# Kernel tuning notes

Hardware: AMD Instinct MI355X
Metric: run time of the kernel (lower is better)

## Reference

```python
import jax, jax.numpy as jnp
import numpy as np

B, S, D, H = 2, 2048, 1024, 16
DK = D // H


def setup_inputs() -> dict:
    key = jax.random.key(0)
    ks = jax.random.split(key, 9)
    sc = 0.02
    return {
        "x": jax.random.normal(ks[0], (B, S, D), dtype=jnp.float32),
        "attention_mask": jnp.ones((B, S), dtype=jnp.int32),
        "Wq": jax.random.normal(ks[1], (D, D), dtype=jnp.float32) * sc,
        "bq": jax.random.normal(ks[2], (D,), dtype=jnp.float32) * sc,
        "Wk": jax.random.normal(ks[3], (D, D), dtype=jnp.float32) * sc,
        "bk": jax.random.normal(ks[4], (D,), dtype=jnp.float32) * sc,
        "Wv": jax.random.normal(ks[5], (D, D), dtype=jnp.float32) * sc,
        "bv": jax.random.normal(ks[6], (D,), dtype=jnp.float32) * sc,
        "Wo": jax.random.normal(ks[7], (D, D), dtype=jnp.float32) * sc,
        "bo": jax.random.normal(ks[8], (D,), dtype=jnp.float32) * sc,
    }


def reference(x, attention_mask, Wq, bq, Wk, bk, Wv, bv, Wo, bo):
    b, s, d = x.shape
    # projections (Linear: x @ W + b) then split heads -> [b, h, s, dk]
    def heads(t):
        return t.reshape(b, s, H, DK).transpose(0, 2, 1, 3)
    Q = heads(x @ Wq + bq)
    K = heads(x @ Wk + bk)
    V = heads(x @ Wv + bv)
    # NOTE: original computes K @ Q^T (not Q @ K^T) and applies NO 1/sqrt(dk) scale
    scores = jnp.einsum("bhid,bhjd->bhij", K, Q)  # [b, h, s, s]
    causal = jnp.tril(jnp.ones((s, s), dtype=bool))  # [s, s]
    final_mask = attention_mask[:, None, None, :].astype(bool) & causal[None, None]
    scores = jnp.where(final_mask, scores, -jnp.inf)
    attn = jax.nn.softmax(scores, axis=-1)
    out = jnp.einsum("bhij,bhjd->bhid", attn, V)  # [b, h, s, dk]
    out = out.transpose(0, 2, 1, 3).reshape(b, s, d)
    return out @ Wo + bo
```

## Files before the change

### kernel.cpp

```cpp
#include <hip/hip_runtime.h>
#include <stdint.h>
#include <stddef.h>


typedef short bf16x8 __attribute__((ext_vector_type(8)));
typedef float f32x4  __attribute__((ext_vector_type(4)));

__device__ __forceinline__ short f2bf(float f) {
  union { float f; uint32_t u; } a; a.f = f;
  uint32_t r = a.u + 0x7fffu + ((a.u >> 16) & 1u);
  return (short)(r >> 16);
}
__device__ __forceinline__ float bf2f(short s) {
  union { uint32_t u; float f; } a; a.u = ((uint32_t)(uint16_t)s) << 16;
  return a.f;
}
__device__ __forceinline__ uint32_t pack2bf(float a, float b) {
  union { float f; uint32_t u; } x, y; x.f = a; y.f = b;
  return (x.u >> 16) | (y.u & 0xffff0000u);
}
__device__ __forceinline__ float fast_exp2(float x) {
#if __has_builtin(__builtin_amdgcn_exp2f)
  return __builtin_amdgcn_exp2f(x);
#else
  return exp2f(x);
#endif
}
__device__ __forceinline__ void async16(const void* g, void* l) {
  __builtin_amdgcn_global_load_lds(
      (const __attribute__((address_space(1))) uint32_t*)g,
      (__attribute__((address_space(3))) uint32_t*)l, 16, 0, 0);
}
#define MFMA(a, b, c) __builtin_amdgcn_mfma_f32_16x16x32_bf16((a), (b), (c), 0, 0, 0)

__global__ void k_prep(const float* __restrict__ x, short* __restrict__ xhi,
                       const float* __restrict__ Wq, const float* __restrict__ Wk,
                       const float* __restrict__ Wv, const float* __restrict__ Wo,
                       short* __restrict__ whi, short* __restrict__ wo) {
  __shared__ float T[64][65];
  int bid = blockIdx.x;
  int t = threadIdx.x;
  if (bid < 4096) {
    int i = bid * 256 + t;
    float4 v = ((const float4*)x)[i];
    short4 h;
    h.x = f2bf(v.x);
    h.y = f2bf(v.y);
    h.z = f2bf(v.z);
    h.w = f2bf(v.w);
    ((short4*)xhi)[i] = h;
  } else {
    int i = bid - 4096;
    int bx = i & 15, by = (i >> 4) & 15, z = i >> 8;
    const float* W = (z == 0) ? Wq : (z == 1) ? Wk : (z == 2) ? Wv : Wo;
    int n0 = bx * 64, k0 = by * 64;
    int rr = t >> 4, cc = (t & 15) * 4;
#pragma unroll
    for (int it = 0; it < 4; ++it) {
      int row = rr + it * 16;
      float4 v = *(const float4*)&W[(size_t)(k0 + row) * 1024 + n0 + cc];
      T[row][cc] = v.x; T[row][cc + 1] = v.y; T[row][cc + 2] = v.z; T[row][cc + 3] = v.w;
    }
    __syncthreads();
    short* oh = (z < 3) ? (whi + (size_t)z * 1048576) : wo;
#pragma unroll
    for (int it = 0; it < 4; ++it) {
      int nrow = rr + it * 16;
      short4 h4;
      h4.x = f2bf(T[cc + 0][nrow]);
      h4.y = f2bf(T[cc + 1][nrow]);
      h4.z = f2bf(T[cc + 2][nrow]);
      h4.w = f2bf(T[cc + 3][nrow]);
      *(short4*)&oh[(size_t)(n0 + nrow) * 1024 + k0 + cc] = h4;
    }
  }
}

__global__ __launch_bounds__(256, 3) void k_gemm_qkv(
    const short* __restrict__ xhi, const short* __restrict__ whi,
    const float* __restrict__ bq, const float* __restrict__ bk,
    const float* __restrict__ bv,
    short* __restrict__ Qhi, short* __restrict__ Qlo,
    short* __restrict__ Khi, short* __restrict__ Klo,
    short* __restrict__ Vt) {
  __shared__ short AH[2][4096];
  __shared__ short BH[2][4096];
  int tid = threadIdx.x;
  int bx = blockIdx.x;
  int m0 = blockIdx.y * 128;
  int n0g = bx * 128;
  int w = tid >> 6, lane = tid & 63, lr = lane & 15, lq = lane >> 4;
  int wm = w >> 1, wn = w & 1;
  int z = bx >> 3;
  f32x4 acc[4][4] = {};

  auto stage = [&](int ks, int pb) {
#pragma unroll
    for (int it = 0; it < 2; ++it) {
      int idx = it * 256 + tid;
      int row = idx >> 2, c = idx & 3;
      int cs = c ^ (row & 3);
      async16(xhi + (size_t)(m0 + row) * 1024 + ks * 32 + cs * 8, &AH[pb][idx * 8]);
      async16(whi + (size_t)(n0g + row) * 1024 + ks * 32 + cs * 8, &BH[pb][idx * 8]);
    }
  };

  stage(0, 0);
  int p = 0;
  int g = lq ^ (lr & 3);
  if (z == 2) {
    for (int ks = 0; ks < 32; ++ks) {
      __syncthreads();
      if (ks < 31) stage(ks + 1, p ^ 1);
      const bf16x8* A8 = (const bf16x8*)AH[p];
      const bf16x8* B8 = (const bf16x8*)BH[p];
      bf16x8 af[4], bfr[4];
#pragma unroll
      for (int mt = 0; mt < 4; ++mt) af[mt] = A8[(wm * 64 + mt * 16 + lr) * 4 + g];
#pragma unroll
      for (int nt = 0; nt < 4; ++nt) bfr[nt] = B8[(wn * 64 + nt * 16 + lr) * 4 + g];
#pragma unroll
      for (int mt = 0; mt < 4; ++mt)
#pragma unroll
        for (int nt = 0; nt < 4; ++nt)
          acc[mt][nt] = MFMA(af[mt], bfr[nt], acc[mt][nt]);
      p ^= 1;
    }
#pragma unroll
    for (int nt = 0; nt < 4; ++nt) {
      int dg = (n0g & 1023) + wn * 64 + nt * 16 + lr;
      float bvv = bv[dg];
      int hh = dg >> 6, dk = dg & 63;
#pragma unroll
      for (int mt = 0; mt < 4; ++mt) {
        int row = m0 + wm * 64 + mt * 16 + lq * 4;
        int b_ = row >> 11, s_ = row & 2047;
        short4 pk;
        pk.x = f2bf(acc[mt][nt][0] + bvv);
        pk.y = f2bf(acc[mt][nt][1] + bvv);
        pk.z = f2bf(acc[mt][nt][2] + bvv);
        pk.w = f2bf(acc[mt][nt][3] + bvv);
        *(short4*)&Vt[(size_t)((b_ * 16 + hh) * 64 + dk) * 2048 + s_] = pk;
      }
    }
  } else {
    for (int ks = 0; ks < 32; ++ks) {
      __syncthreads();
      if (ks < 31) stage(ks + 1, p ^ 1);
      const bf16x8* A8 = (const bf16x8*)AH[p];
      const bf16x8* B8 = (const bf16x8*)BH[p];
      bf16x8 af[4], bfr[4];
#pragma unroll
      for (int mt = 0; mt < 4; ++mt) af[mt] = A8[(wm * 64 + mt * 16 + lr) * 4 + g];
#pragma unroll
      for (int nt = 0; nt < 4; ++nt) bfr[nt] = B8[(wn * 64 + nt * 16 + lr) * 4 + g];
#pragma unroll
      for (int mt = 0; mt < 4; ++mt)
#pragma unroll
        for (int nt = 0; nt < 4; ++nt)
          acc[mt][nt] = MFMA(bfr[nt], af[mt], acc[mt][nt]);
      p ^= 1;
    }
    const float LOG2E = 1.44269504f;
    const float* bias = (z == 0) ? bq : bk;
    short* Ch = (z == 0) ? Qhi : Khi;
    short* Cl = (z == 0) ? Qlo : Klo;
#pragma unroll
    for (int mt = 0; mt < 4; ++mt) {
      int row = m0 + wm * 64 + mt * 16 + lr;
#pragma unroll
      for (int nt = 0; nt < 4; ++nt) {
        int colg = (n0g & 1023) + wn * 64 + nt * 16 + lq * 4;
        float4 b4 = *(const float4*)&bias[colg];
        float v0 = acc[mt][nt][0] + b4.x;
        float v1 = acc[mt][nt][1] + b4.y;
        float v2 = acc[mt][nt][2] + b4.z;
        float v3 = acc[mt][nt][3] + b4.w;
        if (z == 0) { v0 *= LOG2E; v1 *= LOG2E; v2 *= LOG2E; v3 *= LOG2E; }
        short4 hi4, lo4;
        hi4.x = f2bf(v0); lo4.x = f2bf(v0 - bf2f(hi4.x));
        hi4.y = f2bf(v1); lo4.y = f2bf(v1 - bf2f(hi4.y));
        hi4.z = f2bf(v2); lo4.z = f2bf(v2 - bf2f(hi4.z));
        hi4.w = f2bf(v3); lo4.w = f2bf(v3 - bf2f(hi4.w));
        size_t o = (size_t)row * 1024 + colg;
        *(short4*)&Ch[o] = hi4;
        if (z == 1) *(short4*)&Cl[o] = lo4;
      }
    }
  }
}

__global__ __launch_bounds__(256, 3) void k_gemm_o(
    const short* __restrict__ Ab, const short* __restrict__ Bb,
    const float* __restrict__ bias, float* __restrict__ Cf) {
  __shared__ short AH[2][4096];
  __shared__ short BH[2][4096];
  int tid = threadIdx.x;
  int m0 = blockIdx.y * 128, n0 = blockIdx.x * 128;
  int w = tid >> 6, lane = tid & 63, lr = lane & 15, lq = lane >> 4;
  int wm = w >> 1, wn = w & 1;
  f32x4 acc[4][4] = {};

  auto stage = [&](int ks, int pb) {
#pragma unroll
    for (int it = 0; it < 2; ++it) {
      int idx = it * 256 + tid;
      int row = idx >> 2, c = idx & 3;
      int cs = c ^ (row & 3);
      async16(Ab + (size_t)(m0 + row) * 1024 + ks * 32 + cs * 8, &AH[pb][idx * 8]);
      async16(Bb + (size_t)(n0 + row) * 1024 + ks * 32 + cs * 8, &BH[pb][idx * 8]);
    }
  };

  stage(0, 0);
  int p = 0;
  int g = lq ^ (lr & 3);
  for (int ks = 0; ks < 32; ++ks) {
    __syncthreads();
    if (ks < 31) stage(ks + 1, p ^ 1);
    const bf16x8* A8 = (const bf16x8*)AH[p];
    const bf16x8* B8 = (const bf16x8*)BH[p];
    bf16x8 af[4], bfr[4];
#pragma unroll
    for (int mt = 0; mt < 4; ++mt) af[mt] = A8[(wm * 64 + mt * 16 + lr) * 4 + g];
#pragma unroll
    for (int nt = 0; nt < 4; ++nt) bfr[nt] = B8[(wn * 64 + nt * 16 + lr) * 4 + g];
#pragma unroll
    for (int mt = 0; mt < 4; ++mt)
#pragma unroll
      for (int nt = 0; nt < 4; ++nt)
        acc[mt][nt] = MFMA(bfr[nt], af[mt], acc[mt][nt]);
    p ^= 1;
  }

#pragma unroll
  for (int mt = 0; mt < 4; ++mt) {
    int row = m0 + wm * 64 + mt * 16 + lr;
#pragma unroll
    for (int nt = 0; nt < 4; ++nt) {
      int colg = n0 + wn * 64 + nt * 16 + lq * 4;
      float4 b4 = *(const float4*)&bias[colg];
      float4 o4;
      o4.x = acc[mt][nt][0] + b4.x;
      o4.y = acc[mt][nt][1] + b4.y;
      o4.z = acc[mt][nt][2] + b4.z;
      o4.w = acc[mt][nt][3] + b4.w;
      *(float4*)&Cf[(size_t)row * 1024 + colg] = o4;
    }
  }
}

__global__ __launch_bounds__(256, 4) void k_attn(
    const short* __restrict__ Khi, const short* __restrict__ Klo,
    const short* __restrict__ Qhi, const short* __restrict__ Vt,
    const int* __restrict__ amask, short* __restrict__ Obuf,
    float* __restrict__ PA, float* __restrict__ PB,
    float* __restrict__ LA, float* __restrict__ LB) {
  __shared__ short QH[2][4096];
  __shared__ short VS[2][4096];
  int tid = threadIdx.x;
  int bid = blockIdx.x;
  int xcd = bid & 7, i2 = bid >> 3;
  int bh = xcd * 4 + (i2 & 3);
  int o  = i2 >> 2;
  int P, t0, t1;
  bool partial, slotB = false;
  if (o < 16) {
    P = 16 + o; t0 = 0; t1 = 16; partial = true;
  } else {
    int q = o - 16, lvl = q >> 1;
    if (q & 1) {
      P = 15 - lvl; t0 = 0; t1 = P + 1; partial = false;
    } else {
      P = 31 - lvl; t0 = 16; t1 = P + 1; partial = true; slotB = true;
    }
  }
  int b = bh >> 4, h = bh & 15;
  int w = tid >> 6, lane = tid & 63, lr = lane & 15, lq = lane >> 4;
  int band = 2 * P + (w >> 1);
  int rb0 = band * 32 + (w & 1) * 16;

  bf16x8 kh[2], kl[2];
  {
    size_t ra = ((size_t)(b * 2048 + rb0 + lr)) * 1024 + h * 64;
#pragma unroll
    for (int ks = 0; ks < 2; ++ks) {
      kh[ks] = *(const bf16x8*)(Khi + ra + ks * 32 + lq * 8);
      kl[ks] = *(const bf16x8*)(Klo + ra + ks * 32 + lq * 8);
    }
  }

  f32x4 O[4] = {};
  float ls = 0.f;
  int iq = rb0 + lr;
  int baddr0 = (((lq & 1) * 2) * 16 + lr) * 4;
  int baddr1 = baddr0 + 64;

  auto stage = [&](int jt, int pb) {
    int j0 = jt * 64;
#pragma unroll
    for (int it = 0; it < 2; ++it) {
      int idx2 = it * 256 + tid;
      int rr = idx2 >> 3, c = idx2 & 7;
      int cs = c ^ (rr & 7);
      size_t gq = ((size_t)(b * 2048 + j0 + rr)) * 1024 + h * 64 + cs * 8;
      async16(Qhi + gq, &QH[pb][idx2 * 8]);
      size_t gv = ((size_t)(bh * 64 + rr)) * 2048 + j0 + cs * 8;
      async16(Vt + gv, &VS[pb][idx2 * 8]);
    }
  };

  stage(t0, 0);
  int p = 0;
  for (int t = t0; t < t1; ++t) {
    __syncthreads();
    if (t + 1 < t1) stage(t + 1, p ^ 1);
    int j0 = t * 64;
    const bf16x8* Q8 = (const bf16x8*)QH[p];
    const bf16x8* V8 = (const bf16x8*)VS[p];

    int av = amask[b * 2048 + j0 + lane];
    unsigned long long bal = __ballot(av != 0);
    bool allv = (bal == ~0ull);

    f32x4 s[4] = {};
#pragma unroll
    for (int mt = 0; mt < 4; ++mt) {
      int row = mt * 16 + lr;
#pragma unroll
      for (int ks = 0; ks < 2; ++ks) {
        int gi = row * 8 + ((ks * 4 + lq) ^ (row & 7));
        bf16x8 qa = Q8[gi];
        s[mt] = MFMA(qa, kh[ks], s[mt]);
        s[mt] = MFMA(qa, kl[ks], s[mt]);
      }
    }

    bool diag = (t == P);
    float pv[4][4];
#pragma unroll
    for (int mt = 0; mt < 4; ++mt)
#pragma unroll
      for (int r = 0; r < 4; ++r)
        pv[mt][r] = fast_exp2(s[mt][r]);
    if (diag) {
#pragma unroll
      for (int mt = 0; mt < 4; ++mt)
#pragma unroll
        for (int r = 0; r < 4; ++r)
          if (j0 + mt * 16 + lq * 4 + r > iq) pv[mt][r] = 0.f;
    }
    if (!allv) {
#pragma unroll
      for (int mt = 0; mt < 4; ++mt)
#pragma unroll
        for (int r = 0; r < 4; ++r)
          if (!((bal >> (mt * 16 + lq * 4 + r)) & 1)) pv[mt][r] = 0.f;
    }
    uint32_t pd[4][2];
#pragma unroll
    for (int mt = 0; mt < 4; ++mt) {
      ls += (pv[mt][0] + pv[mt][1]) + (pv[mt][2] + pv[mt][3]);
      pd[mt][0] = pack2bf(pv[mt][0], pv[mt][1]);
      pd[mt][1] = pack2bf(pv[mt][2], pv[mt][3]);
    }

#pragma unroll
    for (int k2 = 0; k2 < 2; ++k2) {
      union { int i[4]; bf16x8 v; } pa;
#pragma unroll
      for (int dd = 0; dd < 4; ++dd) {
        int addr = (dd >> 1) ? baddr1 : baddr0;
        int v0 = __builtin_amdgcn_ds_bpermute(addr, (int)pd[k2 * 2 + 0][dd & 1]);
        int v1 = __builtin_amdgcn_ds_bpermute(addr, (int)pd[k2 * 2 + 1][dd & 1]);
        pa.i[dd] = (lq >> 1) ? v1 : v0;
      }
#pragma unroll
      for (int nt = 0; nt < 4; ++nt) {
        int row = nt * 16 + lr;
        bf16x8 vb = V8[row * 8 + ((k2 * 4 + lq) ^ (row & 7))];
        O[nt] = MFMA(pa.v, vb, O[nt]);
      }
    }
    p ^= 1;
  }

  float tsum = ls;
  tsum += __shfl_xor(tsum, 16);
  tsum += __shfl_xor(tsum, 32);

  if (!partial) {
    float inv[4];
#pragma unroll
    for (int r = 0; r < 4; ++r) inv[r] = 1.0f / __shfl(tsum, lq * 4 + r, 64);
#pragma unroll
    for (int nt = 0; nt < 4; ++nt)
#pragma unroll
      for (int r = 0; r < 4; ++r) {
        int row = b * 2048 + rb0 + lq * 4 + r;
        int col = h * 64 + nt * 16 + lr;
        Obuf[(size_t)row * 1024 + col] = f2bf(O[nt][r] * inv[r]);
      }
  } else {
    float* PO = slotB ? PB : PA;
    float* PL = slotB ? LB : LA;
    int prb = bh * 1024 + (P - 16) * 64 + w * 16;
#pragma unroll
    for (int nt = 0; nt < 4; ++nt)
#pragma unroll
      for (int r = 0; r < 4; ++r)
        PO[(size_t)(prb + lq * 4 + r) * 64 + nt * 16 + lr] = O[nt][r];
    if (lq == 0) PL[prb + lr] = tsum;
  }
}

__global__ void k_merge(const float* __restrict__ PA, const float* __restrict__ PB,
                        const float* __restrict__ LA, const float* __restrict__ LB,
                        short* __restrict__ Obuf) {
  int t = blockIdx.x * 256 + threadIdx.x;
  int pr = t >> 4, cg = t & 15;
  float4 a = ((const float4*)PA)[pr * 16 + cg];
  float4 bb4 = ((const float4*)PB)[pr * 16 + cg];
  float inv = 1.0f / (LA[pr] + LB[pr]);
  int bh = pr >> 10, P = 16 + ((pr >> 6) & 15), loc = pr & 63;
  int b = bh >> 4, h = bh & 15;
  size_t addr = ((size_t)(b * 2048 + P * 64 + loc)) * 1024 + h * 64 + cg * 4;
  short4 oq;
  oq.x = f2bf((a.x + bb4.x) * inv);
  oq.y = f2bf((a.y + bb4.y) * inv);
  oq.z = f2bf((a.z + bb4.z) * inv);
  oq.w = f2bf((a.w + bb4.w) * inv);
  *(short4*)&Obuf[addr] = oq;
}

extern "C" void kernel_launch(void* const* d_in, const int* in_sizes, int n_in,
                              void* d_out, int out_size, void* d_ws, size_t ws_size,
                              hipStream_t stream) {
  const float* x  = (const float*)d_in[0];
  const int* amask = (const int*)d_in[1];
  const float* Wq = (const float*)d_in[2];
  const float* bq = (const float*)d_in[3];
  const float* Wk = (const float*)d_in[4];
  const float* bk = (const float*)d_in[5];
  const float* Wv = (const float*)d_in[6];
  const float* bv = (const float*)d_in[7];
  const float* Wo = (const float*)d_in[8];
  const float* bo = (const float*)d_in[9];

  char* ws = (char*)d_ws;
  const size_t MB = 1024 * 1024;
  short* xhi = (short*)(ws);
  float* PA  = (float*)(ws + 8 * MB);
  short* whi = (short*)(ws + 16 * MB);
  float* LA  = (float*)(ws + 22 * MB);
  float* LB  = (float*)(ws + 23 * MB);
  short* wo  = (short*)(ws + 26 * MB);
  short* Qhi = (short*)(ws + 28 * MB);
  float* PB  = (float*)(ws + 36 * MB);
  short* Qlo = (short*)(ws + 36 * MB);
  short* Khi = (short*)(ws + 44 * MB);
  short* Klo = (short*)(ws + 52 * MB);
  short* Vt  = (short*)(ws + 60 * MB);
  short* Obuf = xhi;

  k_prep<<<5120, 256, 0, stream>>>(x, xhi, Wq, Wk, Wv, Wo, whi, wo);
  k_gemm_qkv<<<dim3(24, 32), 256, 0, stream>>>(xhi, whi, bq, bk, bv,
                                               Qhi, Qlo, Khi, Klo, Vt);
  k_attn<<<1536, 256, 0, stream>>>(Khi, Klo, Qhi, Vt, amask, Obuf,
                                   PA, PB, LA, LB);
  k_merge<<<2048, 256, 0, stream>>>(PA, PB, LA, LB, Obuf);
  k_gemm_o<<<dim3(8, 32), 256, 0, stream>>>(Obuf, wo, bo, (float*)d_out);
}
```

Before: 201.9 us.

## Split key tile across warp pairs and reduce partial outputs via LDS

Each warp previously owned 16 query rows (K-rows here) and swept all 64 columns of each tile. Now a warp pair shares 32 rows, with each warp covering half of the 64 j-columns. Each warp holds K fragments for two 16-row groups and reuses each loaded Q/V fragment across both groups, which cuts LDS reads per MFMA. The two halves' O and row sums are combined through an LDS scratch step after the loop. This costs an extra barrier, LDS traffic and more accumulator registers, and the writing warp must wait on its partner.

```diff
diff --git a/kernel.cpp b/kernel.cpp
--- a/kernel.cpp
+++ b/kernel.cpp
@@ -277,22 +277,22 @@
   }
   int b = bh >> 4, h = bh & 15;
   int w = tid >> 6, lane = tid & 63, lr = lane & 15, lq = lane >> 4;
-  int band = 2 * P + (w >> 1);
-  int rb0 = band * 32 + (w & 1) * 16;
-
-  bf16x8 kh[2], kl[2];
-  {
-    size_t ra = ((size_t)(b * 2048 + rb0 + lr)) * 1024 + h * 64;
+  int qh = w >> 1, jh = w & 1;
+  int q0 = P * 64 + qh * 32;
+
+  bf16x8 kh[2][2], kl[2][2];
+#pragma unroll
+  for (int ig = 0; ig < 2; ++ig) {
+    size_t ra = ((size_t)(b * 2048 + q0 + ig * 16 + lr)) * 1024 + h * 64;
 #pragma unroll
     for (int ks = 0; ks < 2; ++ks) {
-      kh[ks] = *(const bf16x8*)(Khi + ra + ks * 32 + lq * 8);
-      kl[ks] = *(const bf16x8*)(Klo + ra + ks * 32 + lq * 8);
-    }
-  }
-
-  f32x4 O[4] = {};
-  float ls = 0.f;
-  int iq = rb0 + lr;
+      kh[ig][ks] = *(const bf16x8*)(Khi + ra + ks * 32 + lq * 8);
+      kl[ig][ks] = *(const bf16x8*)(Klo + ra + ks * 32 + lq * 8);
+    }
+  }
+
+  f32x4 O[2][4] = {};
+  float ls[2] = {0.f, 0.f};
   int baddr0 = (((lq & 1) * 2) * 16 + lr) * 4;
   int baddr1 = baddr0 + 64;
 
@@ -323,94 +323,132 @@
     unsigned long long bal = __ballot(av != 0);
     bool allv = (bal == ~0ull);
 
-    f32x4 s[4] = {};
-#pragma unroll
-    for (int mt = 0; mt < 4; ++mt) {
-      int row = mt * 16 + lr;
+    f32x4 s[2][2] = {};
+#pragma unroll
+    for (int jg = 0; jg < 2; ++jg) {
+      int row = (2 * jh + jg) * 16 + lr;
 #pragma unroll
       for (int ks = 0; ks < 2; ++ks) {
         int gi = row * 8 + ((ks * 4 + lq) ^ (row & 7));
         bf16x8 qa = Q8[gi];
-        s[mt] = MFMA(qa, kh[ks], s[mt]);
-        s[mt] = MFMA(qa, kl[ks], s[mt]);
+#pragma unroll
+        for (int ig = 0; ig < 2; ++ig) {
+          s[jg][ig] = MFMA(qa, kh[ig][ks], s[jg][ig]);
+          s[jg][ig] = MFMA(qa, kl[ig][ks], s[jg][ig]);
+        }
       }
     }
 
     bool diag = (t == P);
-    float pv[4][4];
-#pragma unroll
-    for (int mt = 0; mt < 4; ++mt)
-#pragma unroll
-      for (int r = 0; r < 4; ++r)
-        pv[mt][r] = fast_exp2(s[mt][r]);
-    if (diag) {
-#pragma unroll
-      for (int mt = 0; mt < 4; ++mt)
-#pragma unroll
-        for (int r = 0; r < 4; ++r)
-          if (j0 + mt * 16 + lq * 4 + r > iq) pv[mt][r] = 0.f;
-    }
-    if (!allv) {
-#pragma unroll
-      for (int mt = 0; mt < 4; ++mt)
-#pragma unroll
-        for (int r = 0; r < 4; ++r)
-          if (!((bal >> (mt * 16 + lq * 4 + r)) & 1)) pv[mt][r] = 0.f;
-    }
-    uint32_t pd[4][2];
-#pragma unroll
-    for (int mt = 0; mt < 4; ++mt) {
-      ls += (pv[mt][0] + pv[mt][1]) + (pv[mt][2] + pv[mt][3]);
-      pd[mt][0] = pack2bf(pv[mt][0], pv[mt][1]);
-      pd[mt][1] = pack2bf(pv[mt][2], pv[mt][3]);
-    }
-
-#pragma unroll
-    for (int k2 = 0; k2 < 2; ++k2) {
+    uint32_t pd[2][2][2];
+#pragma unroll
+    for (int jg = 0; jg < 2; ++jg)
+#pragma unroll
+      for (int ig = 0; ig < 2; ++ig) {
+        float pv[4];
+#pragma unroll
+        for (int r = 0; r < 4; ++r) pv[r] = fast_exp2(s[jg][ig][r]);
+        if (diag) {
+          int iq = q0 + ig * 16 + lr;
+#pragma unroll
+          for (int r = 0; r < 4; ++r)
+            if (j0 + (2 * jh + jg) * 16 + lq * 4 + r > iq) pv[r] = 0.f;
+        }
+        if (!allv) {
+#pragma unroll
+          for (int r = 0; r < 4; ++r)
+            if (!((bal >> ((2 * jh + jg) * 16 + lq * 4 + r)) & 1)) pv[r] = 0.f;
+        }
+        ls[ig] += (pv[0] + pv[1]) + (pv[2] + pv[3]);
+        pd[jg][ig][0] = pack2bf(pv[0], pv[1]);
+        pd[jg][ig][1] = pack2bf(pv[2], pv[3]);
+      }
+
+    bf16x8 vb[4];
+#pragma unroll
+    for (int nt = 0; nt < 4; ++nt) {
+      int row = nt * 16 + lr;
+      vb[nt] = V8[row * 8 + ((jh * 4 + lq) ^ (row & 7))];
+    }
+
+#pragma unroll
+    for (int ig = 0; ig < 2; ++ig) {
       union { int i[4]; bf16x8 v; } pa;
 #pragma unroll
       for (int dd = 0; dd < 4; ++dd) {
         int addr = (dd >> 1) ? baddr1 : baddr0;
-        int v0 = __builtin_amdgcn_ds_bpermute(addr, (int)pd[k2 * 2 + 0][dd & 1]);
-        int v1 = __builtin_amdgcn_ds_bpermute(addr, (int)pd[k2 * 2 + 1][dd & 1]);
+        int v0 = __builtin_amdgcn_ds_bpermute(addr, (int)pd[0][ig][dd & 1]);
+        int v1 = __builtin_amdgcn_ds_bpermute(addr, (int)pd[1][ig][dd & 1]);
         pa.i[dd] = (lq >> 1) ? v1 : v0;
       }
 #pragma unroll
-      for (int nt = 0; nt < 4; ++nt) {
-        int row = nt * 16 + lr;
-        bf16x8 vb = V8[row * 8 + ((k2 * 4 + lq) ^ (row & 7))];
-        O[nt] = MFMA(pa.v, vb, O[nt]);
+      for (int nt = 0; nt < 4; ++nt)
+        O[ig][nt] = MFMA(pa.v, vb[nt], O[ig][nt]);
+    }
+    p ^= 1;
+  }
+
+#pragma unroll
+  for (int ig = 0; ig < 2; ++ig) {
+    ls[ig] += __shfl_xor(ls[ig], 16);
+    ls[ig] += __shfl_xor(ls[ig], 32);
+  }
+
+  __syncthreads();
+  float* scr = (qh == 0) ? (float*)&QH[0][0] : (float*)&VS[0][0];
+  if (jh == 0) {
+#pragma unroll
+    for (int ig = 0; ig < 2; ++ig) {
+#pragma unroll
+      for (int nt = 0; nt < 4; ++nt)
+#pragma unroll
+        for (int r = 0; r < 4; ++r)
+          scr[(ig * 16 + lq * 4 + r) * 68 + nt * 16 + lr] = O[ig][nt][r];
+      if (lq == 0) scr[(ig * 16 + lr) * 68 + 64] = ls[ig];
+    }
+  }
+  __syncthreads();
+  if (jh == 1) {
+    float tot[2];
+#pragma unroll
+    for (int ig = 0; ig < 2; ++ig)
+      tot[ig] = ls[ig] + scr[(ig * 16 + lr) * 68 + 64];
+    if (!partial) {
+      float inv[2][4];
+#pragma unroll
+      for (int ig = 0; ig < 2; ++ig)
+#pragma unroll
+        for (int r = 0; r < 4; ++r)
+          inv[ig][r] = 1.0f / __shfl(tot[ig], lq * 4 + r, 64);
+#pragma unroll
+      for (int ig = 0; ig < 2; ++ig)
+#pragma unroll
+        for (int nt = 0; nt < 4; ++nt)
+#pragma unroll
+          for (int r = 0; r < 4; ++r) {
+            float oo = O[ig][nt][r] +
+                       scr[(ig * 16 + lq * 4 + r) * 68 + nt * 16 + lr];
+            int row = b * 2048 + q0 + ig * 16 + lq * 4 + r;
+            int col = h * 64 + nt * 16 + lr;
+            Obuf[(size_t)row * 1024 + col] = f2bf(oo * inv[ig][r]);
+          }
+    } else {
+      float* PO = slotB ? PB : PA;
+      float* PL = slotB ? LB : LA;
+      int prb = bh * 1024 + (P - 16) * 64 + qh * 32;
+#pragma unroll
+      for (int ig = 0; ig < 2; ++ig) {
+#pragma unroll
+        for (int nt = 0; nt < 4; ++nt)
+#pragma unroll
+          for (int r = 0; r < 4; ++r) {
+            float oo = O[ig][nt][r] +
+                       scr[(ig * 16 + lq * 4 + r) * 68 + nt * 16 + lr];
+            PO[(size_t)(prb + ig * 16 + lq * 4 + r) * 64 + nt * 16 + lr] = oo;
+          }
+        if (lq == 0) PL[prb + ig * 16 + lr] = tot[ig];
       }
     }
-    p ^= 1;
-  }
-
-  float tsum = ls;
-  tsum += __shfl_xor(tsum, 16);
-  tsum += __shfl_xor(tsum, 32);
-
-  if (!partial) {
-    float inv[4];
-#pragma unroll
-    for (int r = 0; r < 4; ++r) inv[r] = 1.0f / __shfl(tsum, lq * 4 + r, 64);
-#pragma unroll
-    for (int nt = 0; nt < 4; ++nt)
-#pragma unroll
-      for (int r = 0; r < 4; ++r) {
-        int row = b * 2048 + rb0 + lq * 4 + r;
-        int col = h * 64 + nt * 16 + lr;
-        Obuf[(size_t)row * 1024 + col] = f2bf(O[nt][r] * inv[r]);
-      }
-  } else {
-    float* PO = slotB ? PB : PA;
-    float* PL = slotB ? LB : LA;
-    int prb = bh * 1024 + (P - 16) * 64 + w * 16;
-#pragma unroll
-    for (int nt = 0; nt < 4; ++nt)
-#pragma unroll
-      for (int r = 0; r < 4; ++r)
-        PO[(size_t)(prb + lq * 4 + r) * 64 + nt * 16 + lr] = O[nt][r];
-    if (lq == 0) PL[prb + lr] = tsum;
   }
 }
 
```

Measured after the change: 211.9 us. 1.05x slower.
